# Kernel optimization log

Hardware: AMD Instinct MI355X
Metric: run time of the kernel (lower is better)

## Reference

```python
import jax, jax.numpy as jnp
import numpy as np

VOCAB = 32000
EMBED = 512
NUM_CLASS = 5
LEAVES = 8192
N_NODES = 2 * LEAVES - 1


def _build_tree(n_leaves):
    """Balanced binary tree over n_leaves leaves, nodes listed in post-order
    (children always appear before their parent), matching the recursive
    traversal order of the original torch module."""
    is_leaf, word, left, right = [], [], [], []

    def rec(lo, hi):
        if hi - lo == 1:
            is_leaf.append(1)
            word.append((lo * 2654435761) % VOCAB)
            left.append(0)
            right.append(0)
        else:
            mid = (lo + hi) // 2
            l = rec(lo, mid)
            r = rec(mid, hi)
            is_leaf.append(0)
            word.append(0)
            left.append(l)
            right.append(r)
        return len(is_leaf) - 1

    rec(0, n_leaves)
    return (np.asarray(is_leaf, np.int32), np.asarray(word, np.int32),
            np.asarray(left, np.int32), np.asarray(right, np.int32))


def setup_inputs() -> dict:
    key = jax.random.key(0)
    k1, k2, k3, k4, k5 = jax.random.split(key, 5)
    is_leaf, word, left, right = _build_tree(LEAVES)
    scale = 0.05
    return {
        "is_leaf": jnp.asarray(is_leaf),
        "word": jnp.asarray(word),
        "left": jnp.asarray(left),
        "right": jnp.asarray(right),
        "emb": jax.random.normal(k1, (VOCAB, EMBED), jnp.float32) * scale,
        "W": jax.random.normal(k2, (EMBED, 2 * EMBED), jnp.float32) * scale,
        "bW": jax.random.normal(k3, (EMBED,), jnp.float32) * scale,
        "P": jax.random.normal(k4, (NUM_CLASS, EMBED), jnp.float32) * scale,
        "bP": jax.random.normal(k5, (NUM_CLASS,), jnp.float32) * scale,
    }


def reference(is_leaf, word, left, right, emb, W, bW, P, bP):
    n = is_leaf.shape[0]

    def step(H, xs):
        idx, lf, wd, li, ri = xs
        # internal node: relu(W @ [h_left; h_right] + b)
        pair = jnp.concatenate([H[li], H[ri]])          # [2D]
        internal = pair @ W.T + bW                       # [D]
        leaf = emb[wd]                                   # [D]
        h = jax.nn.relu(jnp.where(lf == 1, leaf, internal))
        return H.at[idx].set(h), None

    H0 = jnp.zeros((n, EMBED), emb.dtype)
    xs = (jnp.arange(n, dtype=jnp.int32), is_leaf, word, left, right)
    H, _ = jax.lax.scan(step, H0, xs)
    # per-node class logits, rows in traversal (post-)order: [N, num_class]
    return H @ P.T + bP
```

## Files before the change

### kernel.cpp

```cpp
#include <hip/hip_runtime.h>


#define EMBED 512
#define K2    1024
#define WOFF  (EMBED * K2)

typedef _Float16 half8 __attribute__((ext_vector_type(8)));
typedef float    floatx4 __attribute__((ext_vector_type(4)));

__device__ __forceinline__ float relu_f(float x) { return fmaxf(x, 0.0f); }

#define GLDS16(gp, lp)                                                        \
    __builtin_amdgcn_global_load_lds(                                         \
        (const __attribute__((address_space(1))) void*)(gp),                  \
        (__attribute__((address_space(3))) void*)(lp), 16, 0, 0)

__global__ __launch_bounds__(256)
void packleaf(const float* __restrict__ W, const float* __restrict__ emb,
              const int* __restrict__ word,
              _Float16* __restrict__ Whp,
              _Float16* __restrict__ Hh, _Float16* __restrict__ Hl,
              int nLeaves)
{
    int tid = threadIdx.x;
    int wave = tid >> 6, lane = tid & 63;

    {
        int t = blockIdx.x * 256 + tid;
        int n = t >> 7, kc = t & 127;
        const float* src = W + (size_t)n * K2 + kc * 8;
        int s = kc >> 2, quad = kc & 3;
        int ln = (quad << 4) | (n & 15);
        size_t off = (size_t)(n >> 4) * 16384 + (size_t)s * 512 + (size_t)ln * 8;
        half8 hi, lo;
#pragma unroll
        for (int j = 0; j < 8; ++j) {
            float w = src[j];
            _Float16 h16 = (_Float16)w;
            hi[j] = h16;
            lo[j] = (_Float16)(w - (float)h16);
        }
        *(half8*)(Whp + off) = hi;
        *(half8*)(Whp + WOFF + off) = lo;
    }
    {
#pragma unroll
        for (int i = 0; i < 8; ++i) {
            int m = blockIdx.x * 32 + wave * 8 + i;
            if (m < nLeaves) {
                int idx = 2 * m - __popc(m);
                int wd = word[idx];
                const float4* src = (const float4*)(emb + (size_t)wd * EMBED) + lane * 2;
                float4 a = src[0], b = src[1];
                float v[8] = {a.x, a.y, a.z, a.w, b.x, b.y, b.z, b.w};
                half8 hi, lo;
#pragma unroll
                for (int j = 0; j < 8; ++j) {
                    float x = relu_f(v[j]);
                    _Float16 h16 = (_Float16)x;
                    hi[j] = h16;
                    lo[j] = (_Float16)(x - (float)h16);
                }
                *(half8*)(Hh + (size_t)idx * EMBED + lane * 8) = hi;
                *(half8*)(Hl + (size_t)idx * EMBED + lane * 8) = lo;
            }
        }
    }
}

__global__ __launch_bounds__(256, 1)
void gemm_big(const _Float16* H,
              const _Float16* __restrict__ Wp,
              const float* __restrict__ bW,
              _Float16* Hh, _Float16* Hl,
              int h, int M, int hoff)
{
    __shared__ _Float16 lds[49152];

    int tid = threadIdx.x;
    int wave = tid >> 6, lane = tid & 63;
    int q = lane >> 4, r = lane & 15;
    int wm = wave >> 1, wn = wave & 1;
    int bm0 = blockIdx.x * 64, bn0 = blockIdx.y * 128;

    int ms = bm0 + wave * 16 + r;
    if (ms >= M) ms = M - 1;
    int node_s = ((ms + 1) << (h + 1)) - 2 - __popc(ms);
    int aL = (node_s - (1 << h)) * EMBED + q * 8;
    int aR = (node_s - 1) * EMBED + q * 8;

    floatx4 acc[2][4];
#pragma unroll
    for (int i = 0; i < 2; ++i)
#pragma unroll
        for (int j = 0; j < 4; ++j) acc[i][j] = (floatx4){0.f, 0.f, 0.f, 0.f};

    for (int kc = 0; kc < 8; ++kc) {
        int abase = ((kc < 4) ? aL : aR) + (kc & 3) * 128;
#pragma unroll
        for (int i = 0; i < 8; ++i) {
            int s2 = i >> 1, hl = i & 1;
            const _Float16* gp = H + abase + s2 * 32 + (hl ? hoff : 0);
            GLDS16(gp, &lds[(wave * 8 + i) * 512]);
        }
#pragma unroll
        for (int j = 0; j < 16; ++j) {
            int u = wave * 2 + (j >> 3), s2 = (j >> 1) & 3, hl = j & 1;
            const _Float16* gp = Wp + (size_t)(blockIdx.y * 8 + u) * 16384
                               + (kc * 4 + s2) * 512 + (hl ? WOFF : 0) + lane * 8;
            GLDS16(gp, &lds[16384 + (wave * 16 + j) * 512]);
        }
        __syncthreads();

#pragma unroll
        for (int s2 = 0; s2 < 4; ++s2) {
            half8 ah[2], al[2], bh[4], bl[4];
#pragma unroll
            for (int t2 = 0; t2 < 2; ++t2) {
                int t = wm * 2 + t2;
                ah[t2] = *(const half8*)&lds[(t * 8 + s2 * 2 + 0) * 512 + lane * 8];
                al[t2] = *(const half8*)&lds[(t * 8 + s2 * 2 + 1) * 512 + lane * 8];
            }
#pragma unroll
            for (int u2 = 0; u2 < 4; ++u2) {
                int u = wn * 4 + u2;
                bh[u2] = *(const half8*)&lds[16384 + (u * 8 + s2 * 2 + 0) * 512 + lane * 8];
                bl[u2] = *(const half8*)&lds[16384 + (u * 8 + s2 * 2 + 1) * 512 + lane * 8];
            }
#pragma unroll
            for (int t2 = 0; t2 < 2; ++t2)
#pragma unroll
                for (int u2 = 0; u2 < 4; ++u2) {
                    acc[t2][u2] = __builtin_amdgcn_mfma_f32_16x16x32_f16(ah[t2], bh[u2], acc[t2][u2], 0, 0, 0);
                    acc[t2][u2] = __builtin_amdgcn_mfma_f32_16x16x32_f16(ah[t2], bl[u2], acc[t2][u2], 0, 0, 0);
                    acc[t2][u2] = __builtin_amdgcn_mfma_f32_16x16x32_f16(al[t2], bh[u2], acc[t2][u2], 0, 0, 0);
                }
        }
        __syncthreads();
    }

#pragma unroll
    for (int t2 = 0; t2 < 2; ++t2)
#pragma unroll
        for (int reg = 0; reg < 4; ++reg) {
            int m = bm0 + (wm * 2 + t2) * 16 + q * 4 + reg;
            if (m < M) {
                int node = ((m + 1) << (h + 1)) - 2 - __popc(m);
#pragma unroll
                for (int u2 = 0; u2 < 4; ++u2) {
                    int col = bn0 + (wn * 4 + u2) * 16 + r;
                    float v = relu_f(acc[t2][u2][reg] + bW[col]);
                    _Float16 hi = (_Float16)v;
                    Hh[(size_t)node * EMBED + col] = hi;
                    Hl[(size_t)node * EMBED + col] = (_Float16)(v - (float)hi);
                }
            }
        }
}

__global__ __launch_bounds__(256)
void gemm_splitk(const _Float16* __restrict__ Hh, const _Float16* __restrict__ Hl,
                 const _Float16* __restrict__ Wp,
                 const float* __restrict__ bW,
                 _Float16* HhO, _Float16* HlO,
                 int h, int M)
{
    __shared__ float red[4 * 256];

    int tid = threadIdx.x;
    int wave = tid >> 6, lane = tid & 63;
    int q = lane >> 4, r = lane & 15;
    int mt = blockIdx.x, u = blockIdx.y;

    int m = mt * 16 + r;
    if (m >= M) m = M - 1;
    int idx = ((m + 1) << (h + 1)) - 2 - __popc(m);
    int childRow = (wave < 2) ? (idx - (1 << h)) : (idx - 1);
    int kbase = (wave & 1) * 256;
    const _Float16* pAh = Hh + (size_t)childRow * EMBED + kbase + q * 8;
    const _Float16* pAl = Hl + (size_t)childRow * EMBED + kbase + q * 8;
    const _Float16* pB  = Wp + (size_t)u * 16384 + (size_t)(wave * 8) * 512 + lane * 8;

    floatx4 acc = (floatx4){0.f, 0.f, 0.f, 0.f};
#pragma unroll
    for (int s = 0; s < 8; ++s) {
        half8 ah = *(const half8*)(pAh + s * 32);
        half8 al = *(const half8*)(pAl + s * 32);
        half8 bh = *(const half8*)(pB + s * 512);
        half8 bl = *(const half8*)(pB + s * 512 + WOFF);
        acc = __builtin_amdgcn_mfma_f32_16x16x32_f16(ah, bh, acc, 0, 0, 0);
        acc = __builtin_amdgcn_mfma_f32_16x16x32_f16(ah, bl, acc, 0, 0, 0);
        acc = __builtin_amdgcn_mfma_f32_16x16x32_f16(al, bh, acc, 0, 0, 0);
    }
#pragma unroll
    for (int reg = 0; reg < 4; ++reg)
        red[wave * 256 + (q * 4 + reg) * 16 + r] = acc[reg];
    __syncthreads();

    int row = tid >> 4, col = tid & 15;
    float v = red[row * 16 + col] + red[256 + row * 16 + col]
            + red[512 + row * 16 + col] + red[768 + row * 16 + col];
    int mm = mt * 16 + row;
    if (mm < M) {
        int node = ((mm + 1) << (h + 1)) - 2 - __popc(mm);
        int colg = u * 16 + col;
        float x = relu_f(v + bW[colg]);
        _Float16 hi = (_Float16)x;
        HhO[(size_t)node * EMBED + colg] = hi;
        HlO[(size_t)node * EMBED + colg] = (_Float16)(x - (float)hi);
    }
}

__global__ __launch_bounds__(256)
void out_kernel(const _Float16* __restrict__ Hh, const _Float16* __restrict__ Hl,
                const float* __restrict__ P, const float* __restrict__ bP,
                float* __restrict__ out, int nNodes)
{
    int t = blockIdx.x * 256 + threadIdx.x;
    int node = t >> 6, lane = t & 63;
    if (node >= nNodes) return;
    half8 hv = *(const half8*)(Hh + (size_t)node * EMBED + lane * 8);
    half8 lv = *(const half8*)(Hl + (size_t)node * EMBED + lane * 8);
    float hx[8];
#pragma unroll
    for (int j = 0; j < 8; ++j) hx[j] = (float)hv[j] + (float)lv[j];
    float s[5];
#pragma unroll
    for (int c = 0; c < 5; ++c) {
        const float* p = P + c * EMBED + lane * 8;
        float4 p0 = *(const float4*)p;
        float4 p1 = *(const float4*)(p + 4);
        s[c] = hx[0] * p0.x + hx[1] * p0.y + hx[2] * p0.z + hx[3] * p0.w
             + hx[4] * p1.x + hx[5] * p1.y + hx[6] * p1.z + hx[7] * p1.w;
    }
#pragma unroll
    for (int o = 32; o > 0; o >>= 1)
#pragma unroll
        for (int c = 0; c < 5; ++c)
            s[c] += __shfl_down(s[c], o, 64);
    if (lane == 0) {
#pragma unroll
        for (int c = 0; c < 5; ++c)
            out[(size_t)node * 5 + c] = s[c] + bP[c];
    }
}

extern "C" void kernel_launch(void* const* d_in, const int* in_sizes, int n_in,
                              void* d_out, int out_size, void* d_ws, size_t ws_size,
                              hipStream_t stream)
{
    const int*   word = (const int*)d_in[1];
    const float* emb  = (const float*)d_in[4];
    const float* W    = (const float*)d_in[5];
    const float* bW   = (const float*)d_in[6];
    const float* P    = (const float*)d_in[7];
    const float* bP   = (const float*)d_in[8];
    float* out = (float*)d_out;

    int nNodes  = in_sizes[0];
    int nLeaves = (nNodes + 1) / 2;

    int hoff = (nNodes + 1) * EMBED;
    _Float16* Hh  = (_Float16*)d_ws;
    _Float16* Hl  = Hh + hoff;
    _Float16* Whp = Hl + hoff;

    packleaf<<<dim3(256), dim3(256), 0, stream>>>(
        W, emb, word, Whp, Hh, Hl, nLeaves);
    for (int h = 1; h <= 4; ++h) {
        int M = 1 << (13 - h);
        gemm_big<<<dim3(M / 64, 4), dim3(256), 0, stream>>>(
            Hh, Whp, bW, Hh, Hl, h, M, hoff);
    }
    for (int h = 5; h <= 13; ++h) {
        int M = 1 << (13 - h);
        gemm_splitk<<<dim3((M + 15) / 16, 32), dim3(256), 0, stream>>>(
            Hh, Hl, Whp, bW, Hh, Hl, h, M);
    }
    out_kernel<<<dim3((nNodes * 64 + 255) / 256), dim3(256), 0, stream>>>(
        Hh, Hl, P, bP, out, nNodes);
}
```

Measured before the change: 273.4 us.

## Replace LDS-tiled gemm_big with split-K 32x32 direct-load kernel for lower levels

For tree levels 1-4, swaps the 64x128 LDS-staged GEMM (one block per CU) for a kernel computing 32x32 output tiles, with K split across the four waves and reduced through shared memory. Operands come straight from global memory into registers, with no LDS staging. This launches far more blocks per level and removes the staging barriers, at the cost of no shared reuse of the W operand across waves and an extra reduction step.

```diff
diff --git a/kernel.cpp b/kernel.cpp
--- a/kernel.cpp
+++ b/kernel.cpp
@@ -6,14 +6,10 @@
 #define WOFF  (EMBED * K2)
 
 typedef _Float16 half8 __attribute__((ext_vector_type(8)));
+typedef _Float16 half4 __attribute__((ext_vector_type(4)));
 typedef float    floatx4 __attribute__((ext_vector_type(4)));
 
 __device__ __forceinline__ float relu_f(float x) { return fmaxf(x, 0.0f); }
-
-#define GLDS16(gp, lp)                                                        \
-    __builtin_amdgcn_global_load_lds(                                         \
-        (const __attribute__((address_space(1))) void*)(gp),                  \
-        (__attribute__((address_space(3))) void*)(lp), 16, 0, 0)
 
 __global__ __launch_bounds__(256)
 void packleaf(const float* __restrict__ W, const float* __restrict__ emb,
@@ -68,94 +64,90 @@
     }
 }
 
-__global__ __launch_bounds__(256, 1)
-void gemm_big(const _Float16* H,
-              const _Float16* __restrict__ Wp,
-              const float* __restrict__ bW,
-              _Float16* Hh, _Float16* Hl,
-              int h, int M, int hoff)
-{
-    __shared__ _Float16 lds[49152];
+__global__ __launch_bounds__(256)
+void gemm_splitk32(const _Float16* __restrict__ Hh, const _Float16* __restrict__ Hl,
+                   const _Float16* __restrict__ Wp,
+                   const float* __restrict__ bW,
+                   _Float16* HhO, _Float16* HlO,
+                   int h, int M)
+{
+    __shared__ float red[4096];
 
     int tid = threadIdx.x;
     int wave = tid >> 6, lane = tid & 63;
     int q = lane >> 4, r = lane & 15;
-    int wm = wave >> 1, wn = wave & 1;
-    int bm0 = blockIdx.x * 64, bn0 = blockIdx.y * 128;
-
-    int ms = bm0 + wave * 16 + r;
-    if (ms >= M) ms = M - 1;
-    int node_s = ((ms + 1) << (h + 1)) - 2 - __popc(ms);
-    int aL = (node_s - (1 << h)) * EMBED + q * 8;
-    int aR = (node_s - 1) * EMBED + q * 8;
-
-    floatx4 acc[2][4];
-#pragma unroll
-    for (int i = 0; i < 2; ++i)
-#pragma unroll
-        for (int j = 0; j < 4; ++j) acc[i][j] = (floatx4){0.f, 0.f, 0.f, 0.f};
-
-    for (int kc = 0; kc < 8; ++kc) {
-        int abase = ((kc < 4) ? aL : aR) + (kc & 3) * 128;
-#pragma unroll
-        for (int i = 0; i < 8; ++i) {
-            int s2 = i >> 1, hl = i & 1;
-            const _Float16* gp = H + abase + s2 * 32 + (hl ? hoff : 0);
-            GLDS16(gp, &lds[(wave * 8 + i) * 512]);
-        }
-#pragma unroll
-        for (int j = 0; j < 16; ++j) {
-            int u = wave * 2 + (j >> 3), s2 = (j >> 1) & 3, hl = j & 1;
-            const _Float16* gp = Wp + (size_t)(blockIdx.y * 8 + u) * 16384
-                               + (kc * 4 + s2) * 512 + (hl ? WOFF : 0) + lane * 8;
-            GLDS16(gp, &lds[16384 + (wave * 16 + j) * 512]);
-        }
-        __syncthreads();
-
-#pragma unroll
-        for (int s2 = 0; s2 < 4; ++s2) {
-            half8 ah[2], al[2], bh[4], bl[4];
-#pragma unroll
-            for (int t2 = 0; t2 < 2; ++t2) {
-                int t = wm * 2 + t2;
-                ah[t2] = *(const half8*)&lds[(t * 8 + s2 * 2 + 0) * 512 + lane * 8];
-                al[t2] = *(const half8*)&lds[(t * 8 + s2 * 2 + 1) * 512 + lane * 8];
+    int m0 = blockIdx.x * 32, n0 = blockIdx.y * 32;
+
+    const _Float16 *pAh[2], *pAl[2];
+#pragma unroll
+    for (int mi = 0; mi < 2; ++mi) {
+        int m = m0 + mi * 16 + r;
+        int idx = ((m + 1) << (h + 1)) - 2 - __popc(m);
+        int childRow = (wave < 2) ? (idx - (1 << h)) : (idx - 1);
+        int kbase = (wave & 1) * 256;
+        pAh[mi] = Hh + (size_t)childRow * EMBED + kbase + q * 8;
+        pAl[mi] = Hl + (size_t)childRow * EMBED + kbase + q * 8;
+    }
+    const _Float16* pB[2];
+#pragma unroll
+    for (int ui = 0; ui < 2; ++ui)
+        pB[ui] = Wp + (size_t)(blockIdx.y * 2 + ui) * 16384
+               + (size_t)(wave * 8) * 512 + lane * 8;
+
+    floatx4 acc[2][2];
+#pragma unroll
+    for (int mi = 0; mi < 2; ++mi)
+#pragma unroll
+        for (int ui = 0; ui < 2; ++ui) acc[mi][ui] = (floatx4){0.f, 0.f, 0.f, 0.f};
+
+#pragma unroll
+    for (int s = 0; s < 8; ++s) {
+        half8 ah[2], al[2], bh[2], bl[2];
+#pragma unroll
+        for (int mi = 0; mi < 2; ++mi) {
+            ah[mi] = *(const half8*)(pAh[mi] + s * 32);
+            al[mi] = *(const half8*)(pAl[mi] + s * 32);
+        }
+#pragma unroll
+        for (int ui = 0; ui < 2; ++ui) {
+            bh[ui] = *(const half8*)(pB[ui] + s * 512);
+            bl[ui] = *(const half8*)(pB[ui] + s * 512 + WOFF);
+        }
+#pragma unroll
+        for (int mi = 0; mi < 2; ++mi)
+#pragma unroll
+            for (int ui = 0; ui < 2; ++ui) {
+                acc[mi][ui] = __builtin_amdgcn_mfma_f32_16x16x32_f16(ah[mi], bh[ui], acc[mi][ui], 0, 0, 0);
+                acc[mi][ui] = __builtin_amdgcn_mfma_f32_16x16x32_f16(ah[mi], bl[ui], acc[mi][ui], 0, 0, 0);
+                acc[mi][ui] = __builtin_amdgcn_mfma_f32_16x16x32_f16(al[mi], bh[ui], acc[mi][ui], 0, 0, 0);
             }
-#pragma unroll
-            for (int u2 = 0; u2 < 4; ++u2) {
-                int u = wn * 4 + u2;
-                bh[u2] = *(const half8*)&lds[16384 + (u * 8 + s2 * 2 + 0) * 512 + lane * 8];
-                bl[u2] = *(const half8*)&lds[16384 + (u * 8 + s2 * 2 + 1) * 512 + lane * 8];
-            }
-#pragma unroll
-            for (int t2 = 0; t2 < 2; ++t2)
-#pragma unroll
-                for (int u2 = 0; u2 < 4; ++u2) {
-                    acc[t2][u2] = __builtin_amdgcn_mfma_f32_16x16x32_f16(ah[t2], bh[u2], acc[t2][u2], 0, 0, 0);
-                    acc[t2][u2] = __builtin_amdgcn_mfma_f32_16x16x32_f16(ah[t2], bl[u2], acc[t2][u2], 0, 0, 0);
-                    acc[t2][u2] = __builtin_amdgcn_mfma_f32_16x16x32_f16(al[t2], bh[u2], acc[t2][u2], 0, 0, 0);
-                }
-        }
-        __syncthreads();
-    }
-
-#pragma unroll
-    for (int t2 = 0; t2 < 2; ++t2)
-#pragma unroll
-        for (int reg = 0; reg < 4; ++reg) {
-            int m = bm0 + (wm * 2 + t2) * 16 + q * 4 + reg;
-            if (m < M) {
-                int node = ((m + 1) << (h + 1)) - 2 - __popc(m);
-#pragma unroll
-                for (int u2 = 0; u2 < 4; ++u2) {
-                    int col = bn0 + (wn * 4 + u2) * 16 + r;
-                    float v = relu_f(acc[t2][u2][reg] + bW[col]);
-                    _Float16 hi = (_Float16)v;
-                    Hh[(size_t)node * EMBED + col] = hi;
-                    Hl[(size_t)node * EMBED + col] = (_Float16)(v - (float)hi);
-                }
-            }
-        }
+    }
+
+#pragma unroll
+    for (int mi = 0; mi < 2; ++mi)
+#pragma unroll
+        for (int ui = 0; ui < 2; ++ui)
+#pragma unroll
+            for (int reg = 0; reg < 4; ++reg)
+                red[wave * 1024 + (mi * 16 + q * 4 + reg) * 32 + ui * 16 + r]
+                    = acc[mi][ui][reg];
+    __syncthreads();
+
+    int row = tid >> 3, c4 = (tid & 7) * 4;
+    int mm = m0 + row;
+    int node = ((mm + 1) << (h + 1)) - 2 - __popc(mm);
+    half4 hi4, lo4;
+#pragma unroll
+    for (int j = 0; j < 4; ++j) {
+        int c = row * 32 + c4 + j;
+        float v = red[c] + red[1024 + c] + red[2048 + c] + red[3072 + c];
+        float x = relu_f(v + bW[n0 + c4 + j]);
+        _Float16 hi = (_Float16)x;
+        hi4[j] = hi;
+        lo4[j] = (_Float16)(x - (float)hi);
+    }
+    *(half4*)(HhO + (size_t)node * EMBED + n0 + c4) = hi4;
+    *(half4*)(HlO + (size_t)node * EMBED + n0 + c4) = lo4;
 }
 
 __global__ __launch_bounds__(256)
@@ -269,8 +261,8 @@
         W, emb, word, Whp, Hh, Hl, nLeaves);
     for (int h = 1; h <= 4; ++h) {
         int M = 1 << (13 - h);
-        gemm_big<<<dim3(M / 64, 4), dim3(256), 0, stream>>>(
-            Hh, Whp, bW, Hh, Hl, h, M, hoff);
+        gemm_splitk32<<<dim3(M / 32, 16), dim3(256), 0, stream>>>(
+            Hh, Hl, Whp, bW, Hh, Hl, h, M);
     }
     for (int h = 5; h <= 13; ++h) {
         int M = 1 << (13 - h);
```

After: 252.8 us. 7.5% less time.
